# Kernel optimization log

Measured on AMD Instinct MI355X. Metric: run time of the kernel, lower is better.

Reference implementation:

```python
import jax, jax.numpy as jnp
import numpy as np

D = 1024

def setup_inputs() -> dict:
    key = jax.random.key(0)
    ks = jax.random.split(key, 7)
    s = 1.0 / np.sqrt(D)  # torch Linear default init scale (uniform bound)
    x = jax.random.normal(ks[0], (4, 2048, D), dtype=jnp.float32)
    Wq = jax.random.uniform(ks[1], (D, D), jnp.float32, -s, s)
    Wk = jax.random.uniform(ks[2], (D, D), jnp.float32, -s, s)
    Wv = jax.random.uniform(ks[3], (D, D), jnp.float32, -s, s)
    bq = jax.random.uniform(ks[4], (D,), jnp.float32, -s, s)
    bk = jax.random.uniform(ks[5], (D,), jnp.float32, -s, s)
    bv = jax.random.uniform(ks[6], (D,), jnp.float32, -s, s)
    return {"x": x, "Wq": Wq, "bq": bq, "Wk": Wk, "bk": bk, "Wv": Wv, "bv": bv}

def reference(x, Wq, bq, Wk, bk, Wv, bv):
    # Linear layers: y = x @ W^T + b (weights stored torch-style [out, in])
    Q = jnp.einsum('bsd,ed->bse', x, Wq) + bq
    K = jnp.einsum('bsd,ed->bse', x, Wk) + bk
    V = jnp.einsum('bsd,ed->bse', x, Wv) + bv
    scale = jnp.sqrt(jnp.asarray(Q.shape[-1], Q.dtype))
    scores = jnp.einsum('bqd,bkd->bqk', Q, K) / scale  # [B, S, S]
    probs = jax.nn.softmax(scores, axis=-1)
    return jnp.einsum('bqk,bkd->bqd', probs, V)
```

## Files before the change

kernel.cpp:

```cpp
#include <hip/hip_runtime.h>


typedef __bf16 bf16x8 __attribute__((ext_vector_type(8)));
typedef float f32x4 __attribute__((ext_vector_type(4)));
typedef unsigned short u16;

__device__ __forceinline__ u16 f2b(float f) {
  union { float f; unsigned u; } a; a.f = f;
  unsigned r = a.u + 0x7fffu + ((a.u >> 16) & 1u);
  return (u16)(r >> 16);
}

__device__ __forceinline__ int xcd_swz(int p) {
  return (p & 7) * 32 + (p >> 3);
}

__global__ __launch_bounds__(256) void cast_all_kernel(const float* __restrict__ x,
                                                       const float* __restrict__ Wq,
                                                       const float* __restrict__ Wk,
                                                       const float* __restrict__ Wv,
                                                       u16* __restrict__ xb,
                                                       u16* __restrict__ Wb) {
  int b = blockIdx.x;
  if (b < 8192) {
    const int i = b * 256 + threadIdx.x;
    float4 v = reinterpret_cast<const float4*>(x)[i];
    reinterpret_cast<ushort4*>(xb)[i] =
        make_ushort4(f2b(v.x), f2b(v.y), f2b(v.z), f2b(v.w));
  } else {
    b -= 8192;
    const int w = b >> 10;
    const float* src = (w == 0) ? Wq : (w == 1) ? Wk : Wv;
    const int i = (b & 1023) * 256 + threadIdx.x;
    float4 v = reinterpret_cast<const float4*>(src)[i];
    reinterpret_cast<ushort4*>(Wb + (size_t)w * 1048576)[i] =
        make_ushort4(f2b(v.x), f2b(v.y), f2b(v.z), f2b(v.w));
  }
}

template <int NT>
__device__ __forceinline__ void core8g0(const char* __restrict__ Ab,
                                        const char* __restrict__ Bb, int lda, int ldb,
                                        char* smem, f32x4* acc) {
  const int tid = threadIdx.x;
  const int wave = tid >> 6, lane = tid & 63;
  const int wr = wave >> 2, wc = wave & 3;
  const int fr = lane & 15, fg = lane >> 4;
  const int rd = (fr * 64 + fg * 16) ^ (((fr >> 3) & 1) << 5);
  const int li = (lane * 16) ^ ((lane >> 5) << 5);
  const int sr = li >> 6, sc2 = li & 63;

  auto STAGE = [&](int kt, int p) {
    const int isB = p & 1, s = p >> 1;
    char* lds = smem + (kt & 1) * 65536 + (isB ? 32768 + s * 16384 : s * 16384);
    const char* gb = isB ? Bb : Ab;
    const int ldx = isB ? ldb : lda;
    const int colOff = kt * 128 + s * 64 + sc2;
    __builtin_amdgcn_global_load_lds(
        (const __attribute__((address_space(1))) void*)(gb + (size_t)(wave * 16 + sr) * ldx + colOff),
        (__attribute__((address_space(3))) void*)(lds + wave * 1024), 16, 0, 0);
    __builtin_amdgcn_global_load_lds(
        (const __attribute__((address_space(1))) void*)(gb + (size_t)((8 + wave) * 16 + sr) * ldx + colOff),
        (__attribute__((address_space(3))) void*)(lds + 8192 + wave * 1024), 16, 0, 0);
  };

#pragma unroll
  for (int p = 0; p < 4; ++p) STAGE(0, p);
  STAGE(1, 0);
  STAGE(1, 1);
  asm volatile("s_waitcnt vmcnt(8)" ::: "memory");
  __builtin_amdgcn_s_barrier();
  __builtin_amdgcn_sched_barrier(0);

  bf16x8 bfr[4];
  for (int kt = 0; kt < NT; ++kt) {
    const char* bufA = smem + (kt & 1) * 65536;
    const char* bufB = bufA + 32768;
#pragma unroll
    for (int p = 0; p < 4; ++p) {
      const int s = p >> 1, j = p & 1;
      bf16x8 afr[4];
      if (j == 0) {
#pragma unroll
        for (int n = 0; n < 4; ++n)
          bfr[n] = *reinterpret_cast<const bf16x8*>(bufB + s * 16384 + (wc * 4 + n) * 1024 + rd);
      }
#pragma unroll
      for (int m = 0; m < 4; ++m)
        afr[m] = *reinterpret_cast<const bf16x8*>(bufA + s * 16384 + (wr * 8 + j * 4 + m) * 1024 + rd);
      if (p < 2) { if (kt + 1 < NT) STAGE(kt + 1, p + 2); }
      else       { if (kt + 2 < NT) STAGE(kt + 2, p - 2); }
      __builtin_amdgcn_s_barrier();
      __builtin_amdgcn_sched_barrier(0);
      __builtin_amdgcn_s_setprio(1);
#pragma unroll
      for (int m = 0; m < 4; ++m)
#pragma unroll
        for (int n = 0; n < 4; ++n)
          acc[(j * 4 + m) * 4 + n] = __builtin_amdgcn_mfma_f32_16x16x32_bf16(
              afr[m], bfr[n], acc[(j * 4 + m) * 4 + n], 0, 0, 0);
      __builtin_amdgcn_s_setprio(0);
      if (p == 1) {
        if (kt < NT - 1) asm volatile("s_waitcnt vmcnt(8)" ::: "memory");
        else asm volatile("s_waitcnt vmcnt(0)" ::: "memory");
      } else if (p == 3) {
        if (kt < NT - 2) asm volatile("s_waitcnt vmcnt(8)" ::: "memory");
        else if (kt == NT - 2) asm volatile("s_waitcnt vmcnt(4)" ::: "memory");
      }
      __builtin_amdgcn_s_barrier();
      __builtin_amdgcn_sched_barrier(0);
    }
  }
}

template <int NT>
__device__ __forceinline__ void core2g1(const char* __restrict__ Ab,
                                        const char* __restrict__ Bb, int lda, int ldb,
                                        char* smem, f32x4* acc) {
  const int tid = threadIdx.x;
  const int wave = tid >> 6, lane = tid & 63;
  const int wr = wave >> 2, wc = wave & 3;
  const int fr = lane & 15, fg = lane >> 4;
  const int rd = (fr * 64 + fg * 16) ^ (((fr >> 3) & 1) << 5);
  const int li = (lane * 16) ^ ((lane >> 5) << 5);
  const int sr = li >> 6, sc2 = li & 63;

  auto STAGE = [&](int kt, int s) {
    char* base = smem + (kt & 1) * 49152;
    const int colOff = kt * 128 + s * 64 + sc2;
    char* ldsA = base + s * 8192;
    __builtin_amdgcn_global_load_lds(
        (const __attribute__((address_space(1))) void*)(Ab + (size_t)(wave * 16 + sr) * lda + colOff),
        (__attribute__((address_space(3))) void*)(ldsA + wave * 1024), 16, 0, 0);
    char* ldsB = base + 16384 + s * 16384;
    __builtin_amdgcn_global_load_lds(
        (const __attribute__((address_space(1))) void*)(Bb + (size_t)(wave * 16 + sr) * ldb + colOff),
        (__attribute__((address_space(3))) void*)(ldsB + wave * 1024), 16, 0, 0);
    __builtin_amdgcn_global_load_lds(
        (const __attribute__((address_space(1))) void*)(Bb + (size_t)((8 + wave) * 16 + sr) * ldb + colOff),
        (__attribute__((address_space(3))) void*)(ldsB + 8192 + wave * 1024), 16, 0, 0);
  };

  STAGE(0, 0);
  STAGE(0, 1);
  asm volatile("s_waitcnt vmcnt(3)" ::: "memory");
  __builtin_amdgcn_s_barrier();
  __builtin_amdgcn_sched_barrier(0);

  for (int kt = 0; kt < NT; ++kt) {
    const char* bufA = smem + (kt & 1) * 49152;
    const char* bufB = bufA + 16384;
#pragma unroll
    for (int s = 0; s < 2; ++s) {
      bf16x8 afr[4], bfr[4];
#pragma unroll
      for (int m = 0; m < 4; ++m)
        afr[m] = *reinterpret_cast<const bf16x8*>(bufA + s * 8192 + (wr * 4 + m) * 1024 + rd);
#pragma unroll
      for (int n = 0; n < 4; ++n)
        bfr[n] = *reinterpret_cast<const bf16x8*>(bufB + s * 16384 + (wc * 4 + n) * 1024 + rd);
      if (kt + 1 < NT) STAGE(kt + 1, s);
      __builtin_amdgcn_s_barrier();
      __builtin_amdgcn_sched_barrier(0);
      __builtin_amdgcn_s_setprio(1);
#pragma unroll
      for (int m = 0; m < 4; ++m)
#pragma unroll
        for (int n = 0; n < 4; ++n)
          acc[m * 4 + n] = __builtin_amdgcn_mfma_f32_16x16x32_bf16(
              afr[m], bfr[n], acc[m * 4 + n], 0, 0, 0);
      __builtin_amdgcn_s_setprio(0);
      if (kt < NT - 1) {
        asm volatile("s_waitcnt vmcnt(3)" ::: "memory");
      } else if (s == 0) {
        asm volatile("s_waitcnt vmcnt(0)" ::: "memory");
      }
      __builtin_amdgcn_s_barrier();
      __builtin_amdgcn_sched_barrier(0);
    }
  }
}

__global__ __launch_bounds__(512, 2) void qkproj_kernel(
    const u16* __restrict__ A, const u16* __restrict__ Bm,
    const float* __restrict__ bq, const float* __restrict__ bk,
    u16* __restrict__ QK) {
  extern __shared__ char smem[];
  const int wk = xcd_swz(blockIdx.x);
  const int bx = wk & 31, by = wk >> 5;
  const int tileM = bx * 256, tileN = by * 256;
  f32x4 acc[32] = {};
  core8g0<16>((const char*)A + (size_t)tileM * 2048,
              (const char*)Bm + (size_t)tileN * 2048, 2048, 2048, smem, acc);
  const int tid = threadIdx.x;
  const int wave = tid >> 6, lane = tid & 63;
  const int wr = wave >> 2, wc = wave & 3, fr = lane & 15, fg = lane >> 4;
  const int w = by >> 2;
  const float* bias = (w == 0) ? bq : bk;
  u16* O = QK + (size_t)w * 8388608;
#pragma unroll
  for (int mi = 0; mi < 8; ++mi) {
    const int r0 = tileM + wr * 128 + mi * 16 + fg * 4;
#pragma unroll
    for (int n = 0; n < 4; ++n) {
      const int cw = (tileN + wc * 64 + n * 16 + fr) & 1023;
      const float bi = bias[cw];
#pragma unroll
      for (int jj = 0; jj < 4; ++jj)
        O[(size_t)(r0 + jj) * 1024 + cw] = f2b(acc[mi * 4 + n][jj] + bi);
    }
  }
}

__global__ __launch_bounds__(512, 2) void vproj_kernel(
    const u16* __restrict__ A, const u16* __restrict__ Bv,
    const float* __restrict__ bvv, u16* __restrict__ Vt) {
  extern __shared__ char smem[];
  const int wk = xcd_swz(blockIdx.x);
  const int bx = wk & 63, by = wk >> 6;
  const int tileM = bx * 128, tileN = by * 256;
  f32x4 acc[16] = {};
  core2g1<16>((const char*)A + (size_t)tileM * 2048,
              (const char*)Bv + (size_t)tileN * 2048, 2048, 2048, smem, acc);
  const int tid = threadIdx.x;
  const int wave = tid >> 6, lane = tid & 63;
  const int wr = wave >> 2, wc = wave & 3, fr = lane & 15, fg = lane >> 4;
#pragma unroll
  for (int mi = 0; mi < 4; ++mi) {
    const int r0 = tileM + wr * 64 + mi * 16 + fg * 4;
    const int b = r0 >> 11, s0 = r0 & 2047;
#pragma unroll
    for (int n = 0; n < 4; ++n) {
      const int cw = (tileN + wc * 64 + n * 16 + fr) & 1023;
      const float bi = bvv[cw];
      ushort4 u = make_ushort4(f2b(acc[mi * 4 + n][0] + bi), f2b(acc[mi * 4 + n][1] + bi),
                               f2b(acc[mi * 4 + n][2] + bi), f2b(acc[mi * 4 + n][3] + bi));
      *reinterpret_cast<ushort4*>(&Vt[(size_t)b * 2097152 + (size_t)cw * 2048 + s0]) = u;
    }
  }
}

__global__ __launch_bounds__(512, 2) void sc8_kernel(const u16* __restrict__ Qb,
                                                     const u16* __restrict__ Kb,
                                                     u16* __restrict__ P,
                                                     float* __restrict__ rowpart) {
  extern __shared__ char smem[];
  const int wk = xcd_swz(blockIdx.x);
  const int bx = wk & 7, by = (wk >> 3) & 7, z = wk >> 6;
  const int tileM = bx * 256, tileN = by * 256;
  f32x4 acc[32] = {};
  core8g0<16>((const char*)Qb + (size_t)z * 4194304 + (size_t)tileM * 2048,
              (const char*)Kb + (size_t)z * 4194304 + (size_t)tileN * 2048, 2048, 2048,
              smem, acc);
  const int tid = threadIdx.x;
  const int wave = tid >> 6, lane = tid & 63;
  const int wr = wave >> 2, wc = wave & 3, fr = lane & 15, fg = lane >> 4;
  float* rs = (float*)smem;
  u16* Po = P + (size_t)z * 4194304 + (size_t)tileM * 2048 + tileN;
#pragma unroll
  for (int mi = 0; mi < 8; ++mi) {
#pragma unroll
    for (int jj = 0; jj < 4; ++jj) {
      const int rl = wr * 128 + mi * 16 + fg * 4 + jj;
      float part = 0.f;
#pragma unroll
      for (int n = 0; n < 4; ++n) {
        float e = __expf(acc[mi * 4 + n][jj] * 0.03125f);
        part += e;
        Po[(size_t)rl * 2048 + wc * 64 + n * 16 + fr] = f2b(e);
      }
      part += __shfl_xor(part, 1);
      part += __shfl_xor(part, 2);
      part += __shfl_xor(part, 4);
      part += __shfl_xor(part, 8);
      if (fr == 0) rs[wc * 256 + rl] = part;
    }
  }
  __syncthreads();
  if (tid < 256) {
    float s = rs[tid] + rs[256 + tid] + rs[512 + tid] + rs[768 + tid];
    rowpart[(size_t)by * 8192 + z * 2048 + tileM + tid] = s;
  }
}

__global__ __launch_bounds__(512, 2) void pv8_kernel(const u16* __restrict__ P,
                                                     const u16* __restrict__ Vt,
                                                     const float* __restrict__ rowpart,
                                                     float* __restrict__ out) {
  extern __shared__ char smem[];
  const int wk = xcd_swz(blockIdx.x);
  const int bx = wk & 15, by = (wk >> 4) & 3, z = wk >> 6;
  const int tileM = bx * 128, tileN = by * 256;
  float* rinv = (float*)(smem + 98304);
  const int tid = threadIdx.x;
  if (tid < 128) {
    float s = 0.f;
#pragma unroll
    for (int t = 0; t < 8; ++t) s += rowpart[t * 8192 + z * 2048 + tileM + tid];
    rinv[tid] = 1.0f / s;
  }
  __builtin_amdgcn_sched_barrier(0);
  f32x4 acc[16] = {};
  core2g1<32>((const char*)P + (size_t)z * 8388608 + (size_t)tileM * 4096,
              (const char*)Vt + (size_t)z * 4194304 + (size_t)tileN * 4096, 4096, 4096,
              smem, acc);
  const int wave = tid >> 6, lane = tid & 63;
  const int wr = wave >> 2, wc = wave & 3, fr = lane & 15, fg = lane >> 4;
  float* O = out + (size_t)z * 2097152;
#pragma unroll
  for (int mi = 0; mi < 4; ++mi) {
#pragma unroll
    for (int jj = 0; jj < 4; ++jj) {
      const int r = wr * 64 + mi * 16 + fg * 4 + jj;
      const float inv = rinv[r];
#pragma unroll
      for (int n = 0; n < 4; ++n)
        O[(size_t)(tileM + r) * 1024 + tileN + wc * 64 + n * 16 + fr] =
            acc[mi * 4 + n][jj] * inv;
    }
  }
}

extern "C" void kernel_launch(void* const* d_in, const int* in_sizes, int n_in,
                              void* d_out, int out_size, void* d_ws, size_t ws_size,
                              hipStream_t stream) {
  if (ws_size < ((size_t)72 << 20)) return;
  const float* x = (const float*)d_in[0];
  const float* Wq = (const float*)d_in[1];
  const float* bq = (const float*)d_in[2];
  const float* Wk = (const float*)d_in[3];
  const float* bk = (const float*)d_in[4];
  const float* Wv = (const float*)d_in[5];
  const float* bv = (const float*)d_in[6];
  char* ws = (char*)d_ws;
  u16* xb = (u16*)(ws);
  u16* Pb = (u16*)(ws);
  u16* Qb = (u16*)(ws + ((size_t)16 << 20));
  u16* Kb = (u16*)(ws + ((size_t)32 << 20));
  u16* Vt = (u16*)(ws + ((size_t)48 << 20));
  u16* Wb = (u16*)(ws + ((size_t)64 << 20));
  float* rowpart = (float*)(ws + ((size_t)70 << 20));
  float* out = (float*)d_out;

  (void)hipFuncSetAttribute((const void*)qkproj_kernel,
                            hipFuncAttributeMaxDynamicSharedMemorySize, 131072);
  (void)hipFuncSetAttribute((const void*)vproj_kernel,
                            hipFuncAttributeMaxDynamicSharedMemorySize, 98304);
  (void)hipFuncSetAttribute((const void*)sc8_kernel,
                            hipFuncAttributeMaxDynamicSharedMemorySize, 131072);
  (void)hipFuncSetAttribute((const void*)pv8_kernel,
                            hipFuncAttributeMaxDynamicSharedMemorySize, 98816);

  cast_all_kernel<<<11264, 256, 0, stream>>>(x, Wq, Wk, Wv, xb, Wb);

  qkproj_kernel<<<256, 512, 131072, stream>>>(xb, Wb, bq, bk, Qb);
  vproj_kernel<<<256, 512, 98304, stream>>>(xb, Wb + 2097152, bv, Vt);

  sc8_kernel<<<256, 512, 131072, stream>>>(Qb, Kb, Pb, rowpart);
  pv8_kernel<<<256, 512, 98816, stream>>>(Pb, Vt, rowpart, out);
}
```

Measured before the change: 156.1 us.

## Shrink QK-projection and score GEMM tiles to 256x128 with 512 blocks

Replaces the 256x256 eight-wave GEMM core with a smaller 256x128 core (waves arranged 4x2, 64-wide K steps, simple double buffering). The QK projection and score kernels now launch 512 blocks with 48KB LDS instead of 256 blocks with 128KB. Row-sum partials grow from 8 to 16 column tiles. The aim is better CU occupancy and more blocks to hide latency, at the cost of lower arithmetic intensity per tile and a less deep pipeline, since each step waits on vmcnt(0).

```diff
diff --git a/kernel.cpp b/kernel.cpp
--- a/kernel.cpp
+++ b/kernel.cpp
@@ -11,9 +11,8 @@
   return (u16)(r >> 16);
 }
 
-__device__ __forceinline__ int xcd_swz(int p) {
-  return (p & 7) * 32 + (p >> 3);
-}
+__device__ __forceinline__ int xcd_swz256(int p) { return (p & 7) * 32 + (p >> 3); }
+__device__ __forceinline__ int xcd_swz512(int p) { return (p & 7) * 64 + (p >> 3); }
 
 __global__ __launch_bounds__(256) void cast_all_kernel(const float* __restrict__ x,
                                                        const float* __restrict__ Wq,
@@ -39,77 +38,60 @@
 }
 
 template <int NT>
-__device__ __forceinline__ void core8g0(const char* __restrict__ Ab,
-                                        const char* __restrict__ Bb, int lda, int ldb,
-                                        char* smem, f32x4* acc) {
-  const int tid = threadIdx.x;
-  const int wave = tid >> 6, lane = tid & 63;
-  const int wr = wave >> 2, wc = wave & 3;
+__device__ __forceinline__ void corew(const char* __restrict__ Ab,
+                                      const char* __restrict__ Bb, int lda, int ldb,
+                                      char* smem, f32x4* acc) {
+  const int tid = threadIdx.x;
+  const int wave = tid >> 6, lane = tid & 63;
+  const int wr = wave >> 1, wc = wave & 1;
   const int fr = lane & 15, fg = lane >> 4;
   const int rd = (fr * 64 + fg * 16) ^ (((fr >> 3) & 1) << 5);
   const int li = (lane * 16) ^ ((lane >> 5) << 5);
   const int sr = li >> 6, sc2 = li & 63;
 
-  auto STAGE = [&](int kt, int p) {
-    const int isB = p & 1, s = p >> 1;
-    char* lds = smem + (kt & 1) * 65536 + (isB ? 32768 + s * 16384 : s * 16384);
-    const char* gb = isB ? Bb : Ab;
-    const int ldx = isB ? ldb : lda;
-    const int colOff = kt * 128 + s * 64 + sc2;
-    __builtin_amdgcn_global_load_lds(
-        (const __attribute__((address_space(1))) void*)(gb + (size_t)(wave * 16 + sr) * ldx + colOff),
-        (__attribute__((address_space(3))) void*)(lds + wave * 1024), 16, 0, 0);
-    __builtin_amdgcn_global_load_lds(
-        (const __attribute__((address_space(1))) void*)(gb + (size_t)((8 + wave) * 16 + sr) * ldx + colOff),
-        (__attribute__((address_space(3))) void*)(lds + 8192 + wave * 1024), 16, 0, 0);
+  auto STAGE = [&](int kt) {
+    char* base = smem + (kt & 1) * 24576;
+    const int colOff = kt * 64 + sc2;
+    __builtin_amdgcn_global_load_lds(
+        (const __attribute__((address_space(1))) void*)(Ab + (size_t)(wave * 16 + sr) * lda + colOff),
+        (__attribute__((address_space(3))) void*)(base + wave * 1024), 16, 0, 0);
+    __builtin_amdgcn_global_load_lds(
+        (const __attribute__((address_space(1))) void*)(Ab + (size_t)((8 + wave) * 16 + sr) * lda + colOff),
+        (__attribute__((address_space(3))) void*)(base + 8192 + wave * 1024), 16, 0, 0);
+    __builtin_amdgcn_global_load_lds(
+        (const __attribute__((address_space(1))) void*)(Bb + (size_t)(wave * 16 + sr) * ldb + colOff),
+        (__attribute__((address_space(3))) void*)(base + 16384 + wave * 1024), 16, 0, 0);
   };
 
-#pragma unroll
-  for (int p = 0; p < 4; ++p) STAGE(0, p);
-  STAGE(1, 0);
-  STAGE(1, 1);
-  asm volatile("s_waitcnt vmcnt(8)" ::: "memory");
+  STAGE(0);
+  asm volatile("s_waitcnt vmcnt(0)" ::: "memory");
   __builtin_amdgcn_s_barrier();
   __builtin_amdgcn_sched_barrier(0);
 
-  bf16x8 bfr[4];
   for (int kt = 0; kt < NT; ++kt) {
-    const char* bufA = smem + (kt & 1) * 65536;
-    const char* bufB = bufA + 32768;
-#pragma unroll
-    for (int p = 0; p < 4; ++p) {
-      const int s = p >> 1, j = p & 1;
-      bf16x8 afr[4];
-      if (j == 0) {
-#pragma unroll
-        for (int n = 0; n < 4; ++n)
-          bfr[n] = *reinterpret_cast<const bf16x8*>(bufB + s * 16384 + (wc * 4 + n) * 1024 + rd);
-      }
-#pragma unroll
-      for (int m = 0; m < 4; ++m)
-        afr[m] = *reinterpret_cast<const bf16x8*>(bufA + s * 16384 + (wr * 8 + j * 4 + m) * 1024 + rd);
-      if (p < 2) { if (kt + 1 < NT) STAGE(kt + 1, p + 2); }
-      else       { if (kt + 2 < NT) STAGE(kt + 2, p - 2); }
-      __builtin_amdgcn_s_barrier();
-      __builtin_amdgcn_sched_barrier(0);
-      __builtin_amdgcn_s_setprio(1);
-#pragma unroll
-      for (int m = 0; m < 4; ++m)
-#pragma unroll
-        for (int n = 0; n < 4; ++n)
-          acc[(j * 4 + m) * 4 + n] = __builtin_amdgcn_mfma_f32_16x16x32_bf16(
-              afr[m], bfr[n], acc[(j * 4 + m) * 4 + n], 0, 0, 0);
-      __builtin_amdgcn_s_setprio(0);
-      if (p == 1) {
-        if (kt < NT - 1) asm volatile("s_waitcnt vmcnt(8)" ::: "memory");
-        else asm volatile("s_waitcnt vmcnt(0)" ::: "memory");
-      } else if (p == 3) {
-        if (kt < NT - 2) asm volatile("s_waitcnt vmcnt(8)" ::: "memory");
-        else if (kt == NT - 2) asm volatile("s_waitcnt vmcnt(4)" ::: "memory");
-      }
-      __builtin_amdgcn_s_barrier();
-      __builtin_amdgcn_sched_barrier(0);
-    }
+    const char* bufA = smem + (kt & 1) * 24576;
+    const char* bufB = bufA + 16384;
+    bf16x8 afr[4], bfr[4];
+#pragma unroll
+    for (int m = 0; m < 4; ++m)
+      afr[m] = *reinterpret_cast<const bf16x8*>(bufA + (wr * 4 + m) * 1024 + rd);
+#pragma unroll
+    for (int n = 0; n < 4; ++n)
+      bfr[n] = *reinterpret_cast<const bf16x8*>(bufB + (wc * 4 + n) * 1024 + rd);
+    if (kt + 1 < NT) STAGE(kt + 1);
+    __builtin_amdgcn_s_barrier();
+    __builtin_amdgcn_sched_barrier(0);
+    __builtin_amdgcn_s_setprio(1);
+#pragma unroll
+    for (int m = 0; m < 4; ++m)
+#pragma unroll
+      for (int n = 0; n < 4; ++n)
+        acc[m * 4 + n] = __builtin_amdgcn_mfma_f32_16x16x32_bf16(
+            afr[m], bfr[n], acc[m * 4 + n], 0, 0, 0);
+    __builtin_amdgcn_s_setprio(0);
+    if (kt + 1 < NT) asm volatile("s_waitcnt vmcnt(0)" ::: "memory");
+    __builtin_amdgcn_s_barrier();
+    __builtin_amdgcn_sched_barrier(0);
   }
 }
 
@@ -186,21 +168,21 @@
     const float* __restrict__ bq, const float* __restrict__ bk,
     u16* __restrict__ QK) {
   extern __shared__ char smem[];
-  const int wk = xcd_swz(blockIdx.x);
-  const int bx = wk & 31, by = wk >> 5;
-  const int tileM = bx * 256, tileN = by * 256;
-  f32x4 acc[32] = {};
-  core8g0<16>((const char*)A + (size_t)tileM * 2048,
-              (const char*)Bm + (size_t)tileN * 2048, 2048, 2048, smem, acc);
-  const int tid = threadIdx.x;
-  const int wave = tid >> 6, lane = tid & 63;
-  const int wr = wave >> 2, wc = wave & 3, fr = lane & 15, fg = lane >> 4;
-  const int w = by >> 2;
+  const int wk = xcd_swz512(blockIdx.x);
+  const int bx = wk >> 4, by = wk & 15;
+  const int tileM = bx * 256, tileN = by * 128;
+  f32x4 acc[16] = {};
+  corew<32>((const char*)A + (size_t)tileM * 2048,
+            (const char*)Bm + (size_t)tileN * 2048, 2048, 2048, smem, acc);
+  const int tid = threadIdx.x;
+  const int wave = tid >> 6, lane = tid & 63;
+  const int wr = wave >> 1, wc = wave & 1, fr = lane & 15, fg = lane >> 4;
+  const int w = by >> 3;
   const float* bias = (w == 0) ? bq : bk;
   u16* O = QK + (size_t)w * 8388608;
 #pragma unroll
-  for (int mi = 0; mi < 8; ++mi) {
-    const int r0 = tileM + wr * 128 + mi * 16 + fg * 4;
+  for (int mi = 0; mi < 4; ++mi) {
+    const int r0 = tileM + wr * 64 + mi * 16 + fg * 4;
 #pragma unroll
     for (int n = 0; n < 4; ++n) {
       const int cw = (tileN + wc * 64 + n * 16 + fr) & 1023;
@@ -216,7 +198,7 @@
     const u16* __restrict__ A, const u16* __restrict__ Bv,
     const float* __restrict__ bvv, u16* __restrict__ Vt) {
   extern __shared__ char smem[];
-  const int wk = xcd_swz(blockIdx.x);
+  const int wk = xcd_swz256(blockIdx.x);
   const int bx = wk & 63, by = wk >> 6;
   const int tileM = bx * 128, tileN = by * 256;
   f32x4 acc[16] = {};
@@ -245,23 +227,23 @@
                                                      u16* __restrict__ P,
                                                      float* __restrict__ rowpart) {
   extern __shared__ char smem[];
-  const int wk = xcd_swz(blockIdx.x);
-  const int bx = wk & 7, by = (wk >> 3) & 7, z = wk >> 6;
-  const int tileM = bx * 256, tileN = by * 256;
-  f32x4 acc[32] = {};
-  core8g0<16>((const char*)Qb + (size_t)z * 4194304 + (size_t)tileM * 2048,
-              (const char*)Kb + (size_t)z * 4194304 + (size_t)tileN * 2048, 2048, 2048,
-              smem, acc);
-  const int tid = threadIdx.x;
-  const int wave = tid >> 6, lane = tid & 63;
-  const int wr = wave >> 2, wc = wave & 3, fr = lane & 15, fg = lane >> 4;
+  const int wk = xcd_swz512(blockIdx.x);
+  const int z = wk >> 7, bx = (wk >> 4) & 7, by = wk & 15;
+  const int tileM = bx * 256, tileN = by * 128;
+  f32x4 acc[16] = {};
+  corew<32>((const char*)Qb + (size_t)z * 4194304 + (size_t)tileM * 2048,
+            (const char*)Kb + (size_t)z * 4194304 + (size_t)tileN * 2048, 2048, 2048,
+            smem, acc);
+  const int tid = threadIdx.x;
+  const int wave = tid >> 6, lane = tid & 63;
+  const int wr = wave >> 1, wc = wave & 1, fr = lane & 15, fg = lane >> 4;
   float* rs = (float*)smem;
   u16* Po = P + (size_t)z * 4194304 + (size_t)tileM * 2048 + tileN;
 #pragma unroll
-  for (int mi = 0; mi < 8; ++mi) {
+  for (int mi = 0; mi < 4; ++mi) {
 #pragma unroll
     for (int jj = 0; jj < 4; ++jj) {
-      const int rl = wr * 128 + mi * 16 + fg * 4 + jj;
+      const int rl = wr * 64 + mi * 16 + fg * 4 + jj;
       float part = 0.f;
 #pragma unroll
       for (int n = 0; n < 4; ++n) {
@@ -278,7 +260,7 @@
   }
   __syncthreads();
   if (tid < 256) {
-    float s = rs[tid] + rs[256 + tid] + rs[512 + tid] + rs[768 + tid];
+    float s = rs[tid] + rs[256 + tid];
     rowpart[(size_t)by * 8192 + z * 2048 + tileM + tid] = s;
   }
 }
@@ -288,7 +270,7 @@
                                                      const float* __restrict__ rowpart,
                                                      float* __restrict__ out) {
   extern __shared__ char smem[];
-  const int wk = xcd_swz(blockIdx.x);
+  const int wk = xcd_swz256(blockIdx.x);
   const int bx = wk & 15, by = (wk >> 4) & 3, z = wk >> 6;
   const int tileM = bx * 128, tileN = by * 256;
   float* rinv = (float*)(smem + 98304);
@@ -296,7 +278,7 @@
   if (tid < 128) {
     float s = 0.f;
 #pragma unroll
-    for (int t = 0; t < 8; ++t) s += rowpart[t * 8192 + z * 2048 + tileM + tid];
+    for (int t = 0; t < 16; ++t) s += rowpart[t * 8192 + z * 2048 + tileM + tid];
     rinv[tid] = 1.0f / s;
   }
   __builtin_amdgcn_sched_barrier(0);
@@ -343,19 +325,19 @@
   float* out = (float*)d_out;
 
   (void)hipFuncSetAttribute((const void*)qkproj_kernel,
-                            hipFuncAttributeMaxDynamicSharedMemorySize, 131072);
+                            hipFuncAttributeMaxDynamicSharedMemorySize, 49152);
   (void)hipFuncSetAttribute((const void*)vproj_kernel,
                             hipFuncAttributeMaxDynamicSharedMemorySize, 98304);
   (void)hipFuncSetAttribute((const void*)sc8_kernel,
-                            hipFuncAttributeMaxDynamicSharedMemorySize, 131072);
+                            hipFuncAttributeMaxDynamicSharedMemorySize, 49152);
   (void)hipFuncSetAttribute((const void*)pv8_kernel,
                             hipFuncAttributeMaxDynamicSharedMemorySize, 98816);
 
   cast_all_kernel<<<11264, 256, 0, stream>>>(x, Wq, Wk, Wv, xb, Wb);
 
-  qkproj_kernel<<<256, 512, 131072, stream>>>(xb, Wb, bq, bk, Qb);
+  qkproj_kernel<<<512, 512, 49152, stream>>>(xb, Wb, bq, bk, Qb);
   vproj_kernel<<<256, 512, 98304, stream>>>(xb, Wb + 2097152, bv, Vt);
 
-  sc8_kernel<<<256, 512, 131072, stream>>>(Qb, Kb, Pb, rowpart);
+  sc8_kernel<<<512, 512, 49152, stream>>>(Qb, Kb, Pb, rowpart);
   pv8_kernel<<<256, 512, 98816, stream>>>(Pb, Vt, rowpart, out);
 }
```

Measured after the change: 156.2 us. About the same (+0.0%).
